# Optimization experiments

Measured on AMD Instinct MI355X. Metric: run time of the kernel, lower is better.

Reference implementation:

```python
import jax, jax.numpy as jnp
import numpy as np

IH, IW = 48, 48           # img_size
C = 256                   # inp == oup
NH, HD = 8, 32            # num_heads, head_dims; inner_dim = 256
HID = 4 * C               # MLP hidden
N = IH * IW               # window size (seq len) = 2304
SCALE = (C // NH) ** -0.5 # (inp_dims // num_heads) ** -0.5
EPS = 1e-5


def _relative_position_index():
    coords = np.stack(np.meshgrid(np.arange(IH), np.arange(IW), indexing='ij'))
    cf = coords.reshape(2, -1)
    rel = (cf[:, :, None] - cf[:, None, :]).transpose(1, 2, 0)
    rel[:, :, 0] += IH - 1
    rel[:, :, 1] += IW - 1
    rel[:, :, 0] *= 2 * IW - 1
    return jnp.asarray(rel.sum(-1).astype(np.int32))  # [N, N]


def setup_inputs() -> dict:
    key = jax.random.key(0)
    ks = jax.random.split(key, 12)
    s = 0.02
    return {
        'x': jax.random.normal(ks[0], (1, IH, IW, C), jnp.float32),
        'gamma1': jnp.ones((C,), jnp.float32),
        'beta1': jnp.zeros((C,), jnp.float32),
        'w_qkv': jax.random.normal(ks[1], (C, 3 * NH * HD), jnp.float32) * s,
        'w_proj': jax.random.normal(ks[2], (NH * HD, C), jnp.float32) * s,
        'b_proj': jnp.zeros((C,), jnp.float32),
        'bias_table': jax.random.normal(ks[3], ((2 * IH - 1) * (2 * IW - 1), NH), jnp.float32) * s,
        'gamma2': jnp.ones((C,), jnp.float32),
        'beta2': jnp.zeros((C,), jnp.float32),
        'w_fc1': jax.random.normal(ks[4], (C, HID), jnp.float32) * s,
        'b_fc1': jnp.zeros((HID,), jnp.float32),
        'w_fc2': jax.random.normal(ks[5], (HID, C), jnp.float32) * s,
        'b_fc2': jnp.zeros((C,), jnp.float32),
        'rel_idx': _relative_position_index(),
    }


def _layernorm(x, g, b):
    mu = jnp.mean(x, axis=-1, keepdims=True)
    var = jnp.mean(jnp.square(x - mu), axis=-1, keepdims=True)
    return (x - mu) * jax.lax.rsqrt(var + EPS) * g + b


def reference(x, gamma1, beta1, w_qkv, w_proj, b_proj, bias_table,
              gamma2, beta2, w_fc1, b_fc1, w_fc2, b_fc2, rel_idx):
    shortcut = x                                   # [1, IH, IW, C]
    t = x.reshape(1, N, C)
    t = _layernorm(t, gamma1, beta1)

    # qkv: [1, N, 3*NH*HD] -> q, k, v each [1, NH, N, HD]
    qkv = (t @ w_qkv).reshape(1, N, 3, NH, HD).transpose(2, 0, 3, 1, 4)
    q, k, v = qkv[0], qkv[1], qkv[2]
    q = q * SCALE

    attn = jnp.einsum('bhnd,bhmd->bhnm', q, k)     # [1, NH, N, N]
    # relative position bias: gather table rows by index -> [NH, N, N]
    bias = bias_table[rel_idx.reshape(-1)].reshape(N, N, NH).transpose(2, 0, 1)
    attn = jax.nn.softmax(attn + bias[None], axis=-1)

    o = jnp.einsum('bhnm,bhmd->bhnd', attn, v)     # [1, NH, N, HD]
    o = o.transpose(0, 2, 1, 3).reshape(1, N, NH * HD)
    o = o @ w_proj + b_proj                        # [1, N, C]

    x = shortcut + o.reshape(1, IH, IW, C)
    shortcut = x

    t = _layernorm(x.reshape(1, N, C), gamma2, beta2)
    t = jax.nn.gelu(t @ w_fc1 + b_fc1, approximate=False) @ w_fc2 + b_fc2
    return shortcut + t.reshape(1, IH, IW, C)
```

## Files before the change

kernel.cpp:

```cpp
#include <hip/hip_runtime.h>
#include <hip/hip_bf16.h>
#include <math.h>

#define IH 48
#define IW 48
#define NN 2304
#define CC 256
#define NH 8
#define HD 32
#define HID 1024
#define NBIAS 9025
#define SCALE 0.17677669529663687f
#define LOG2E 1.4426950408889634f
#define LN_EPS 1e-5f

typedef __attribute__((ext_vector_type(8))) short bf16x8;
typedef __attribute__((ext_vector_type(4))) float f32x4;

__device__ __forceinline__ short f2b(float f) {
    __hip_bfloat16 h = __float2bfloat16(f);
    short s; __builtin_memcpy(&s, &h, 2); return s;
}
__device__ __forceinline__ float b2f(short s) {
    __hip_bfloat16 h; __builtin_memcpy(&h, &s, 2); return __bfloat162float(h);
}
__device__ __forceinline__ float fast_exp2(float x) {
#if __has_builtin(__builtin_amdgcn_exp2f)
    return __builtin_amdgcn_exp2f(x);
#else
    return exp2f(x);
#endif
}

__global__ void prep_kernel(const float* __restrict__ x, const float* __restrict__ g,
                            const float* __restrict__ b, short* __restrict__ t1,
                            const float* __restrict__ bt, short* __restrict__ o_bias,
                            const float* __restrict__ w_qkv, const float* __restrict__ w_proj,
                            const float* __restrict__ w_fc1, const float* __restrict__ w_fc2,
                            short* __restrict__ o_qkv, short* __restrict__ o_proj,
                            short* __restrict__ o_fc1, short* __restrict__ o_fc2)
{
    __shared__ float tsh[32][33];
    __shared__ float red[8];
    const int bid = blockIdx.x, tid = threadIdx.x;
    if (bid < NN) {
        float v = x[bid * CC + tid];
        float s = v, s2 = v * v;
        #pragma unroll
        for (int off = 32; off > 0; off >>= 1) {
            s  += __shfl_xor(s, off);
            s2 += __shfl_xor(s2, off);
        }
        const int wid = tid >> 6;
        if ((tid & 63) == 0) { red[wid * 2] = s; red[wid * 2 + 1] = s2; }
        __syncthreads();
        float tot  = red[0] + red[2] + red[4] + red[6];
        float tot2 = red[1] + red[3] + red[5] + red[7];
        float mu   = tot * (1.0f / CC);
        float var  = tot2 * (1.0f / CC) - mu * mu;
        float rstd = rsqrtf(var + LN_EPS);
        t1[bid * CC + tid] = f2b((v - mu) * rstd * g[tid] + b[tid]);
        return;
    }
    if (bid < NN + 768) {
        int bb = bid - NN;
        const float* src; short* dst; int K, Nn, kt, nt;
        if (bb < 192)      { src = w_qkv;  dst = o_qkv;  K = 256;  Nn = 768;  kt = bb / 24; nt = bb % 24; }
        else if (bb < 256) { bb -= 192; src = w_proj; dst = o_proj; K = 256;  Nn = 256;  kt = bb / 8;  nt = bb % 8; }
        else if (bb < 512) { bb -= 256; src = w_fc1;  dst = o_fc1;  K = 256;  Nn = 1024; kt = bb / 32; nt = bb % 32; }
        else               { bb -= 512; src = w_fc2;  dst = o_fc2;  K = 1024; Nn = 256;  kt = bb / 8;  nt = bb % 8; }
        const int r = tid >> 5, c = tid & 31;
        const int k0 = kt * 32, n0 = nt * 32;
        #pragma unroll
        for (int i = 0; i < 4; ++i)
            tsh[r + i * 8][c] = src[(k0 + r + i * 8) * Nn + n0 + c];
        __syncthreads();
        #pragma unroll
        for (int i = 0; i < 4; ++i)
            dst[(n0 + r + i * 8) * K + k0 + c] = f2b(tsh[c][r + i * 8]);
        return;
    }
    const int stride = (gridDim.x - NN - 768) * 256;
    for (int i = (bid - NN - 768) * 256 + tid; i < NBIAS * NH; i += stride) {
        int idx = i >> 3, h = i & 7;
        o_bias[h * NBIAS + idx] = f2b(bt[i] * LOG2E);
    }
}

__global__ void ln_kernel(const float* __restrict__ x,
                          const float* __restrict__ g,
                          const float* __restrict__ b,
                          short* __restrict__ out)
{
    __shared__ float red[8];
    const int row = blockIdx.x, tid = threadIdx.x;
    float v = x[row * CC + tid];
    float s = v, s2 = v * v;
    #pragma unroll
    for (int off = 32; off > 0; off >>= 1) {
        s  += __shfl_xor(s, off);
        s2 += __shfl_xor(s2, off);
    }
    const int wid = tid >> 6;
    if ((tid & 63) == 0) { red[wid * 2] = s; red[wid * 2 + 1] = s2; }
    __syncthreads();
    float tot  = red[0] + red[2] + red[4] + red[6];
    float tot2 = red[1] + red[3] + red[5] + red[7];
    float mu   = tot * (1.0f / CC);
    float var  = tot2 * (1.0f / CC) - mu * mu;
    float rstd = rsqrtf(var + LN_EPS);
    out[row * CC + tid] = f2b((v - mu) * rstd * g[tid] + b[tid]);
}

#define GSTRIDE 72
template<int KLEN, int KSTR, int TM>
__device__ __forceinline__ void mfma_gemm_core(const short* __restrict__ A,
                                               const short* __restrict__ BT,
                                               int m0, int n0, int kb, f32x4 acc[4],
                                               short* lds)
{
    short* As = lds;
    short* Bs = lds + TM * GSTRIDE;
    const int tid  = threadIdx.x;
    const int w    = tid >> 6, lane = tid & 63;
    const int quad = lane >> 4, l15 = lane & 15;
    const int sr = tid >> 2;
    const int sc = (tid & 3) * 16;
    #pragma unroll
    for (int c = 0; c < 4; ++c) acc[c] = (f32x4){0.f, 0.f, 0.f, 0.f};

    const short* Ap = &A [(m0 + sr) * KSTR + kb + sc];
    const short* Bp = &BT[(n0 + sr) * KSTR + kb + sc];
    bf16x8 ra0 = *(const bf16x8*)Ap,       ra1 = *(const bf16x8*)(Ap + 8);
    bf16x8 rb0 = *(const bf16x8*)Bp,       rb1 = *(const bf16x8*)(Bp + 8);
    bf16x8 rc0, rc1;
    const short* Bp2 = Bp;
    if constexpr (TM == 32) {
        Bp2 = &BT[(n0 + sr + 32) * KSTR + kb + sc];
        rc0 = *(const bf16x8*)Bp2;  rc1 = *(const bf16x8*)(Bp2 + 8);
    }

    for (int k0 = 0; k0 < KLEN; k0 += 64) {
        __syncthreads();
        *(bf16x8*)&As[sr * GSTRIDE + sc]     = ra0;
        *(bf16x8*)&As[sr * GSTRIDE + sc + 8] = ra1;
        *(bf16x8*)&Bs[sr * GSTRIDE + sc]     = rb0;
        *(bf16x8*)&Bs[sr * GSTRIDE + sc + 8] = rb1;
        if constexpr (TM == 32) {
            *(bf16x8*)&Bs[(sr + 32) * GSTRIDE + sc]     = rc0;
            *(bf16x8*)&Bs[(sr + 32) * GSTRIDE + sc + 8] = rc1;
        }
        if (k0 + 64 < KLEN) {
            ra0 = *(const bf16x8*)(Ap + k0 + 64);
            ra1 = *(const bf16x8*)(Ap + k0 + 72);
            rb0 = *(const bf16x8*)(Bp + k0 + 64);
            rb1 = *(const bf16x8*)(Bp + k0 + 72);
            if constexpr (TM == 32) {
                rc0 = *(const bf16x8*)(Bp2 + k0 + 64);
                rc1 = *(const bf16x8*)(Bp2 + k0 + 72);
            }
        }
        __syncthreads();
        #pragma unroll
        for (int s = 0; s < 2; ++s) {
            bf16x8 a = *(const bf16x8*)&As[(w * 16 + l15) * GSTRIDE + s * 32 + quad * 8];
            #pragma unroll
            for (int c = 0; c < 4; ++c) {
                bf16x8 b = *(const bf16x8*)&Bs[(c * 16 + l15) * GSTRIDE + s * 32 + quad * 8];
                acc[c] = __builtin_amdgcn_mfma_f32_16x16x32_bf16(a, b, acc[c], 0, 0, 0);
            }
        }
    }
}

__global__ void qkv_kernel(const short* __restrict__ t1, const short* __restrict__ wT,
                           short* __restrict__ qb, short* __restrict__ kb,
                           short* __restrict__ vT)
{
    __shared__ short lds[2 * 64 * GSTRIDE];
    f32x4 acc[4];
    const int m0 = blockIdx.y * 64, n0 = blockIdx.x * 64;
    mfma_gemm_core<256, 256, 64>(t1, wT, m0, n0, 0, acc, lds);
    const int lane = threadIdx.x & 63, w = threadIdx.x >> 6;
    const int quad = lane >> 4, l15 = lane & 15;
    #pragma unroll
    for (int c = 0; c < 4; ++c) {
        int col = n0 + c * 16 + l15;
        int three = col >> 8, rem = col & 255;
        int h = rem >> 5, d = rem & 31;
        #pragma unroll
        for (int r = 0; r < 4; ++r) {
            int row = m0 + w * 16 + quad * 4 + r;
            float v = acc[c][r];
            if (three == 0)      qb[(h * NN + row) * HD + d] = f2b(v * (SCALE * LOG2E));
            else if (three == 1) kb[(h * NN + row) * HD + d] = f2b(v);
            else                 vT[(h * HD + d) * NN + row] = f2b(v);
        }
    }
}

#define PSTRIDE 40
__global__ __launch_bounds__(256) void attn_kernel(
        const short* __restrict__ qb, const short* __restrict__ kb,
        const short* __restrict__ vT, const short* __restrict__ biasT,
        short* __restrict__ o)
{
    __shared__ float Ored[4][16][33];
    __shared__ float lred[4][16];
    __shared__ short sbuf[4][16 * PSTRIDE];
    __shared__ short bwin[48][64];
    const int w = threadIdx.x >> 6, lane = threadIdx.x & 63;
    const int quad = lane >> 4, l15 = lane & 15;
    const int h = blockIdx.x / 144, q0 = (blockIdx.x % 144) * 16;
    const int t0 = w * 576;
    short* sb = &sbuf[w][0];
    const short* bt = &biasT[h * NBIAS];

    const int qi = q0 / IW, qj0 = q0 % IW;

    for (int idx = threadIdx.x; idx < 48 * 63; idx += 256) {
        int kr = idx / 63, cc = idx - kr * 63;
        bwin[kr][cc] = bt[(qi - kr + 47) * 95 + qj0 + cc];
    }

    bf16x8 qf = *(const bf16x8*)&qb[(h * NN + q0 + l15) * HD + quad * 8];

    f32x4 O0 = (f32x4){0.f,0.f,0.f,0.f}, O1 = (f32x4){0.f,0.f,0.f,0.f};
    float lp[4] = {0.f, 0.f, 0.f, 0.f};
    const f32x4 zero = (f32x4){0.f,0.f,0.f,0.f};

    __syncthreads();

    for (int c = 0; c < 18; ++c) {
        const int t = t0 + c * 32;
        bf16x8 k0f = *(const bf16x8*)&kb[(h * NN + t      + l15) * HD + quad * 8];
        bf16x8 k1f = *(const bf16x8*)&kb[(h * NN + t + 16 + l15) * HD + quad * 8];
        f32x4 s0 = __builtin_amdgcn_mfma_f32_16x16x32_bf16(qf, k0f, zero, 0, 0, 0);
        f32x4 s1 = __builtin_amdgcn_mfma_f32_16x16x32_bf16(qf, k1f, zero, 0, 0, 0);
        bf16x8 v0 = *(const bf16x8*)&vT[(h * HD + l15)      * NN + t + quad * 8];
        bf16x8 v1 = *(const bf16x8*)&vT[(h * HD + 16 + l15) * NN + t + quad * 8];

        const int ki0 = t / IW,        kj0_ = t - ki0 * IW;
        const int ki1 = (t + 16) / IW, kj1_ = (t + 16) - ki1 * IW;
        const int cA = quad * 4 + 47 - kj0_ - l15;
        const int cB = quad * 4 + 47 - kj1_ - l15;

        #pragma unroll
        for (int r = 0; r < 4; ++r) {
            float p0 = fast_exp2(s0[r] + b2f(bwin[ki0][cA + r]));
            float p1 = fast_exp2(s1[r] + b2f(bwin[ki1][cB + r]));
            lp[r] += p0 + p1;
            sb[(quad * 4 + r) * PSTRIDE + l15]      = f2b(p0);
            sb[(quad * 4 + r) * PSTRIDE + 16 + l15] = f2b(p1);
        }
        asm volatile("s_waitcnt lgkmcnt(0)" ::: "memory");
        bf16x8 pa = *(const bf16x8*)&sb[l15 * PSTRIDE + quad * 8];
        O0 = __builtin_amdgcn_mfma_f32_16x16x32_bf16(pa, v0, O0, 0, 0, 0);
        O1 = __builtin_amdgcn_mfma_f32_16x16x32_bf16(pa, v1, O1, 0, 0, 0);
    }

    #pragma unroll
    for (int r = 0; r < 4; ++r) {
        float l = lp[r];
        l += __shfl_xor(l, 1); l += __shfl_xor(l, 2);
        l += __shfl_xor(l, 4); l += __shfl_xor(l, 8);
        if (l15 == 0) lred[w][quad * 4 + r] = l;
        Ored[w][quad * 4 + r][l15]      = O0[r];
        Ored[w][quad * 4 + r][16 + l15] = O1[r];
    }
    __syncthreads();
    {
        const int col = threadIdx.x & 31;
        for (int rr = threadIdx.x >> 5; rr < 16; rr += 8) {
            float s = 0.f, l = 0.f;
            #pragma unroll
            for (int pw = 0; pw < 4; ++pw) { s += Ored[pw][rr][col]; l += lred[pw][rr]; }
            o[(q0 + rr) * CC + h * HD + col] = f2b(s / l);
        }
    }
}

__global__ void proj_kernel(const short* __restrict__ o, const short* __restrict__ wT,
                            const float* __restrict__ bias, const float* __restrict__ x_in,
                            float* __restrict__ x2)
{
    __shared__ short lds[(32 + 64) * GSTRIDE];
    f32x4 acc[4];
    const int m0 = blockIdx.y * 32, n0 = blockIdx.x * 64;
    mfma_gemm_core<256, 256, 32>(o, wT, m0, n0, 0, acc, lds);
    const int lane = threadIdx.x & 63, w = threadIdx.x >> 6;
    const int quad = lane >> 4, l15 = lane & 15;
    #pragma unroll
    for (int c = 0; c < 4; ++c) {
        int col = n0 + c * 16 + l15;
        #pragma unroll
        for (int r = 0; r < 4; ++r) {
            int row = m0 + w * 16 + quad * 4 + r;
            x2[row * CC + col] = acc[c][r] + bias[col] + x_in[row * CC + col];
        }
    }
}

__global__ void fc1_kernel(const short* __restrict__ t2, const short* __restrict__ wT,
                           const float* __restrict__ bias, short* __restrict__ h1)
{
    __shared__ short lds[2 * 64 * GSTRIDE];
    f32x4 acc[4];
    const int m0 = blockIdx.y * 64, n0 = blockIdx.x * 64;
    mfma_gemm_core<256, 256, 64>(t2, wT, m0, n0, 0, acc, lds);
    const int lane = threadIdx.x & 63, w = threadIdx.x >> 6;
    const int quad = lane >> 4, l15 = lane & 15;
    #pragma unroll
    for (int c = 0; c < 4; ++c) {
        int col = n0 + c * 16 + l15;
        #pragma unroll
        for (int r = 0; r < 4; ++r) {
            int row = m0 + w * 16 + quad * 4 + r;
            float v = acc[c][r] + bias[col];
            float ge = 0.5f * v * (1.0f + erff(v * 0.7071067811865476f));
            h1[row * HID + col] = f2b(ge);
        }
    }
}

__global__ void fc2_kernel(const short* __restrict__ h1, const short* __restrict__ wT,
                           const float* __restrict__ bias, const float* __restrict__ x2,
                           float* __restrict__ out)
{
    __shared__ short lds[(32 + 64) * GSTRIDE];
    f32x4 acc[4];
    const int m0 = blockIdx.y * 32, n0 = blockIdx.x * 64;
    mfma_gemm_core<1024, 1024, 32>(h1, wT, m0, n0, 0, acc, lds);
    const int lane = threadIdx.x & 63, w = threadIdx.x >> 6;
    const int quad = lane >> 4, l15 = lane & 15;
    #pragma unroll
    for (int c = 0; c < 4; ++c) {
        int col = n0 + c * 16 + l15;
        #pragma unroll
        for (int r = 0; r < 4; ++r) {
            int row = m0 + w * 16 + quad * 4 + r;
            out[row * CC + col] = acc[c][r] + bias[col] + x2[row * CC + col];
        }
    }
}

extern "C" void kernel_launch(void* const* d_in, const int* in_sizes, int n_in,
                              void* d_out, int out_size, void* d_ws, size_t ws_size,
                              hipStream_t stream)
{
    const float* x          = (const float*)d_in[0];
    const float* gamma1     = (const float*)d_in[1];
    const float* beta1      = (const float*)d_in[2];
    const float* w_qkv      = (const float*)d_in[3];
    const float* w_proj     = (const float*)d_in[4];
    const float* b_proj     = (const float*)d_in[5];
    const float* bias_table = (const float*)d_in[6];
    const float* gamma2     = (const float*)d_in[7];
    const float* beta2      = (const float*)d_in[8];
    const float* w_fc1      = (const float*)d_in[9];
    const float* b_fc1      = (const float*)d_in[10];
    const float* w_fc2      = (const float*)d_in[11];
    const float* b_fc2      = (const float*)d_in[12];

    short* S = (short*)d_ws;
    const int NC = NN * CC;
    short* t1     = S;
    short* qb     = t1  + NC;
    short* kb     = qb  + NC;
    short* vT     = kb  + NC;
    short* obuf   = vT  + NC;
    short* t2     = obuf+ NC;
    short* h1     = t2  + NC;
    short* wTqkv  = h1  + NN * HID;
    short* wTproj = wTqkv  + 768 * 256;
    short* wTfc1  = wTproj + 256 * 256;
    short* wTfc2  = wTfc1  + 1024 * 256;
    short* biasT  = wTfc2  + 256 * 1024;
    float* x2     = (float*)(biasT + NH * NBIAS + 8);

    prep_kernel<<<NN + 768 + 64, 256, 0, stream>>>(x, gamma1, beta1, t1,
                                                   bias_table, biasT,
                                                   w_qkv, w_proj, w_fc1, w_fc2,
                                                   wTqkv, wTproj, wTfc1, wTfc2);
    qkv_kernel<<<dim3(12, 36), 256, 0, stream>>>(t1, wTqkv, qb, kb, vT);
    attn_kernel<<<1152, 256, 0, stream>>>(qb, kb, vT, biasT, obuf);
    proj_kernel<<<dim3(4, 72), 128, 0, stream>>>(obuf, wTproj, b_proj, x, x2);
    ln_kernel<<<NN, 256, 0, stream>>>(x2, gamma2, beta2, t2);
    fc1_kernel<<<dim3(16, 36), 256, 0, stream>>>(t2, wTfc1, b_fc1, h1);
    fc2_kernel<<<dim3(4, 72), 128, 0, stream>>>(h1, wTfc2, b_fc2, x2,
                                                (float*)d_out);
}
```

Measured before the change: 161.0 us.

## Split attention keys across two blocks and merge partials in projection GEMM

The attention kernel now splits the key range in two (a split-K over the sequence, in the style of flash-decoding) using a second grid dimension. Each block writes unnormalized fp32 partial outputs and row sums instead of a normalized bf16 result. The projection kernel is rewritten to load both partials, add them, scale by the reciprocal of the combined row sum, convert to bf16 and stage into LDS before the MFMA GEMM. This doubles the attention grid and halves the per-block serial loop and bias window, at the cost of extra fp32 partial traffic and a custom GEMM loader. There is no max subtraction, so the partials combine by simple addition.

```diff
diff --git a/kernel.cpp b/kernel.cpp
--- a/kernel.cpp
+++ b/kernel.cpp
@@ -203,24 +203,25 @@
 __global__ __launch_bounds__(256) void attn_kernel(
         const short* __restrict__ qb, const short* __restrict__ kb,
         const short* __restrict__ vT, const short* __restrict__ biasT,
-        short* __restrict__ o)
+        float* __restrict__ Opart, float* __restrict__ lpart)
 {
     __shared__ float Ored[4][16][33];
     __shared__ float lred[4][16];
     __shared__ short sbuf[4][16 * PSTRIDE];
-    __shared__ short bwin[48][64];
+    __shared__ short bwin[24][64];
     const int w = threadIdx.x >> 6, lane = threadIdx.x & 63;
     const int quad = lane >> 4, l15 = lane & 15;
+    const int sp = blockIdx.y;
     const int h = blockIdx.x / 144, q0 = (blockIdx.x % 144) * 16;
-    const int t0 = w * 576;
+    const int t0 = sp * 1152 + w * 288;
     short* sb = &sbuf[w][0];
     const short* bt = &biasT[h * NBIAS];
 
     const int qi = q0 / IW, qj0 = q0 % IW;
 
-    for (int idx = threadIdx.x; idx < 48 * 63; idx += 256) {
+    for (int idx = threadIdx.x; idx < 24 * 63; idx += 256) {
         int kr = idx / 63, cc = idx - kr * 63;
-        bwin[kr][cc] = bt[(qi - kr + 47) * 95 + qj0 + cc];
+        bwin[kr][cc] = bt[(qi - (sp * 24 + kr) + 47) * 95 + qj0 + cc];
     }
 
     bf16x8 qf = *(const bf16x8*)&qb[(h * NN + q0 + l15) * HD + quad * 8];
@@ -231,7 +232,7 @@
 
     __syncthreads();
 
-    for (int c = 0; c < 18; ++c) {
+    for (int c = 0; c < 9; ++c) {
         const int t = t0 + c * 32;
         bf16x8 k0f = *(const bf16x8*)&kb[(h * NN + t      + l15) * HD + quad * 8];
         bf16x8 k1f = *(const bf16x8*)&kb[(h * NN + t + 16 + l15) * HD + quad * 8];
@@ -240,8 +241,8 @@
         bf16x8 v0 = *(const bf16x8*)&vT[(h * HD + l15)      * NN + t + quad * 8];
         bf16x8 v1 = *(const bf16x8*)&vT[(h * HD + 16 + l15) * NN + t + quad * 8];
 
-        const int ki0 = t / IW,        kj0_ = t - ki0 * IW;
-        const int ki1 = (t + 16) / IW, kj1_ = (t + 16) - ki1 * IW;
+        const int ki0 = t / IW - sp * 24,        kj0_ = t % IW;
+        const int ki1 = (t + 16) / IW - sp * 24, kj1_ = (t + 16) % IW;
         const int cA = quad * 4 + 47 - kj0_ - l15;
         const int cB = quad * 4 + 47 - kj1_ - l15;
 
@@ -275,21 +276,87 @@
             float s = 0.f, l = 0.f;
             #pragma unroll
             for (int pw = 0; pw < 4; ++pw) { s += Ored[pw][rr][col]; l += lred[pw][rr]; }
-            o[(q0 + rr) * CC + h * HD + col] = f2b(s / l);
-        }
-    }
-}
-
-__global__ void proj_kernel(const short* __restrict__ o, const short* __restrict__ wT,
-                            const float* __restrict__ bias, const float* __restrict__ x_in,
-                            float* __restrict__ x2)
+            Opart[sp * (NN * CC) + (q0 + rr) * CC + h * HD + col] = s;
+            if (col == 0) lpart[sp * (NH * NN) + h * NN + q0 + rr] = l;
+        }
+    }
+}
+
+__global__ __launch_bounds__(128) void proj_kernel(
+        const float* __restrict__ Op, const float* __restrict__ lp,
+        const short* __restrict__ wT, const float* __restrict__ bias,
+        const float* __restrict__ x_in, float* __restrict__ x2)
 {
     __shared__ short lds[(32 + 64) * GSTRIDE];
+    __shared__ float rcpl[32][8];
+    short* As = lds;
+    short* Bs = lds + 32 * GSTRIDE;
+    const int tid = threadIdx.x;
+    const int w = tid >> 6, lane = tid & 63;
+    const int quad = lane >> 4, l15 = lane & 15;
+    const int m0 = blockIdx.y * 32, n0 = blockIdx.x * 64;
+    const int sr = tid >> 2, sc = (tid & 3) * 16;
+
+    for (int i = tid; i < 256; i += 128) {
+        int rl = i >> 3, hh = i & 7;
+        float l = lp[hh * NN + m0 + rl] + lp[NH * NN + hh * NN + m0 + rl];
+        rcpl[rl][hh] = 1.0f / l;
+    }
+
     f32x4 acc[4];
-    const int m0 = blockIdx.y * 32, n0 = blockIdx.x * 64;
-    mfma_gemm_core<256, 256, 32>(o, wT, m0, n0, 0, acc, lds);
-    const int lane = threadIdx.x & 63, w = threadIdx.x >> 6;
-    const int quad = lane >> 4, l15 = lane & 15;
+    #pragma unroll
+    for (int c = 0; c < 4; ++c) acc[c] = (f32x4){0.f, 0.f, 0.f, 0.f};
+
+    const float* Ap0 = &Op[(m0 + sr) * CC + sc];
+    const float* Ap1 = Ap0 + NN * CC;
+    f32x4 a0[4], a1[4];
+    #pragma unroll
+    for (int j = 0; j < 4; ++j) {
+        a0[j] = *(const f32x4*)(Ap0 + j * 4);
+        a1[j] = *(const f32x4*)(Ap1 + j * 4);
+    }
+    const short* Bp  = &wT[(n0 + sr) * CC + sc];
+    const short* Bp2 = &wT[(n0 + sr + 32) * CC + sc];
+    bf16x8 rb0 = *(const bf16x8*)Bp,  rb1 = *(const bf16x8*)(Bp + 8);
+    bf16x8 rc0 = *(const bf16x8*)Bp2, rc1 = *(const bf16x8*)(Bp2 + 8);
+
+    for (int k0 = 0; k0 < 256; k0 += 64) {
+        __syncthreads();
+        float r = rcpl[sr][(k0 + sc) >> 5];
+        bf16x8 lo, hi;
+        #pragma unroll
+        for (int j = 0; j < 8; ++j) {
+            lo[j] = f2b((a0[j >> 2][j & 3] + a1[j >> 2][j & 3]) * r);
+            hi[j] = f2b((a0[2 + (j >> 2)][j & 3] + a1[2 + (j >> 2)][j & 3]) * r);
+        }
+        *(bf16x8*)&As[sr * GSTRIDE + sc]     = lo;
+        *(bf16x8*)&As[sr * GSTRIDE + sc + 8] = hi;
+        *(bf16x8*)&Bs[sr * GSTRIDE + sc]     = rb0;
+        *(bf16x8*)&Bs[sr * GSTRIDE + sc + 8] = rb1;
+        *(bf16x8*)&Bs[(sr + 32) * GSTRIDE + sc]     = rc0;
+        *(bf16x8*)&Bs[(sr + 32) * GSTRIDE + sc + 8] = rc1;
+        if (k0 + 64 < 256) {
+            #pragma unroll
+            for (int j = 0; j < 4; ++j) {
+                a0[j] = *(const f32x4*)(Ap0 + k0 + 64 + j * 4);
+                a1[j] = *(const f32x4*)(Ap1 + k0 + 64 + j * 4);
+            }
+            rb0 = *(const bf16x8*)(Bp + k0 + 64);
+            rb1 = *(const bf16x8*)(Bp + k0 + 72);
+            rc0 = *(const bf16x8*)(Bp2 + k0 + 64);
+            rc1 = *(const bf16x8*)(Bp2 + k0 + 72);
+        }
+        __syncthreads();
+        #pragma unroll
+        for (int s = 0; s < 2; ++s) {
+            bf16x8 a = *(const bf16x8*)&As[(w * 16 + l15) * GSTRIDE + s * 32 + quad * 8];
+            #pragma unroll
+            for (int c = 0; c < 4; ++c) {
+                bf16x8 b = *(const bf16x8*)&Bs[(c * 16 + l15) * GSTRIDE + s * 32 + quad * 8];
+                acc[c] = __builtin_amdgcn_mfma_f32_16x16x32_bf16(a, b, acc[c], 0, 0, 0);
+            }
+        }
+    }
     #pragma unroll
     for (int c = 0; c < 4; ++c) {
         int col = n0 + c * 16 + l15;
@@ -368,8 +435,7 @@
     short* qb     = t1  + NC;
     short* kb     = qb  + NC;
     short* vT     = kb  + NC;
-    short* obuf   = vT  + NC;
-    short* t2     = obuf+ NC;
+    short* t2     = vT  + NC;
     short* h1     = t2  + NC;
     short* wTqkv  = h1  + NN * HID;
     short* wTproj = wTqkv  + 768 * 256;
@@ -377,14 +443,16 @@
     short* wTfc2  = wTfc1  + 1024 * 256;
     short* biasT  = wTfc2  + 256 * 1024;
     float* x2     = (float*)(biasT + NH * NBIAS + 8);
+    float* Opart  = x2 + NC;
+    float* lpart  = Opart + 2 * NC;
 
     prep_kernel<<<NN + 768 + 64, 256, 0, stream>>>(x, gamma1, beta1, t1,
                                                    bias_table, biasT,
                                                    w_qkv, w_proj, w_fc1, w_fc2,
                                                    wTqkv, wTproj, wTfc1, wTfc2);
     qkv_kernel<<<dim3(12, 36), 256, 0, stream>>>(t1, wTqkv, qb, kb, vT);
-    attn_kernel<<<1152, 256, 0, stream>>>(qb, kb, vT, biasT, obuf);
-    proj_kernel<<<dim3(4, 72), 128, 0, stream>>>(obuf, wTproj, b_proj, x, x2);
+    attn_kernel<<<dim3(1152, 2), 256, 0, stream>>>(qb, kb, vT, biasT, Opart, lpart);
+    proj_kernel<<<dim3(4, 72), 128, 0, stream>>>(Opart, lpart, wTproj, b_proj, x, x2);
     ln_kernel<<<NN, 256, 0, stream>>>(x2, gamma2, beta2, t2);
     fc1_kernel<<<dim3(16, 36), 256, 0, stream>>>(t2, wTfc1, b_fc1, h1);
     fc2_kernel<<<dim3(4, 72), 128, 0, stream>>>(h1, wTfc2, b_fc2, x2,
```

After: 165.1 us. +2.6%, slower.
